# Optimization experiments

Measured on AMD Instinct MI355X. Metric: run time of the kernel, lower is better.

Reference implementation:

```python
import jax, jax.numpy as jnp
import numpy as np

N, IN, OUT, T = 32768, 512, 512, 8


def setup_inputs() -> dict:
    key = jax.random.key(0)
    k1, k2, k3 = jax.random.split(key, 3)
    x = jax.random.normal(k1, (N, IN), dtype=jnp.float32)
    x_type = jax.random.randint(k2, (N,), 0, T, dtype=jnp.int32)
    # xavier_uniform with relu gain, per torch reset_parameters
    gain = np.sqrt(2.0)
    bound = gain * np.sqrt(6.0 / (IN + OUT))
    W = jax.random.uniform(k3, (T, IN, OUT), dtype=jnp.float32,
                           minval=-bound, maxval=bound)
    return {"x": x, "x_type": x_type, "W": W}


def reference(x, x_type, W):
    # gather_mm semantics: out[i] = x[i] @ W[x_type[i]]
    # Expressed as a small fixed loop over types (T=8) with masking, which
    # avoids materializing the [N, IN, OUT] gathered weight tensor.
    num_types = W.shape[0]
    out = jnp.zeros((x.shape[0], W.shape[2]), dtype=x.dtype)
    for t in range(num_types):
        mask = (x_type == t)[:, None]  # [N, 1]
        out = out + jnp.where(mask, x @ W[t], jnp.zeros((), dtype=x.dtype))
    return out
```

## Files before the change

### kernel.cpp

```cpp
#include <hip/hip_runtime.h>
#include <hip/hip_bf16.h>

#define N_ROWS 32768
#define K_DIM 512
#define OUT_DIM 512
#define N_TYPES 8
#define NB 520
#define BM 64
#define BN 256
#define BK 64

typedef __attribute__((ext_vector_type(8))) short bf16x8;
typedef __attribute__((ext_vector_type(4))) float f32x4;

__device__ inline ushort f2bf(float f) {
    __hip_bfloat16 h = __float2bfloat16(f);
    return *reinterpret_cast<ushort*>(&h);
}

__device__ inline void gload_lds16(const void* g, void* l) {
    __builtin_amdgcn_global_load_lds(
        (const __attribute__((address_space(1))) void*)g,
        (__attribute__((address_space(3))) void*)l, 16, 0, 0);
}

__global__ void k_init(int* meta) {
    if (threadIdx.x < 32) meta[threadIdx.x] = 0;
}

__global__ void k_hist(const int* __restrict__ x_type, int* meta) {
    __shared__ int cnt[N_TYPES];
    if (threadIdx.x < N_TYPES) cnt[threadIdx.x] = 0;
    __syncthreads();
    int i = blockIdx.x * 256 + threadIdx.x;
    atomicAdd(&cnt[x_type[i]], 1);
    __syncthreads();
    if (threadIdx.x < N_TYPES && cnt[threadIdx.x] > 0)
        atomicAdd(&meta[threadIdx.x], cnt[threadIdx.x]);
}

__global__ void k_scan(int* meta) {
    if (threadIdx.x == 0) {
        int s = 0;
        for (int t = 0; t < N_TYPES; ++t) {
            meta[8 + t]  = s;
            meta[20 + t] = s;
            s += (meta[t] + 63) & ~63;
        }
        meta[16] = s;
    }
}

__global__ void k_fill(const int* __restrict__ x_type, int* meta, int* __restrict__ row_ids) {
    __shared__ int lcnt[N_TYPES];
    __shared__ int lbase[N_TYPES];
    if (threadIdx.x < N_TYPES) lcnt[threadIdx.x] = 0;
    __syncthreads();
    int i = blockIdx.x * 256 + threadIdx.x;
    int t = x_type[i];
    int lpos = atomicAdd(&lcnt[t], 1);
    __syncthreads();
    if (threadIdx.x < N_TYPES)
        lbase[threadIdx.x] = (lcnt[threadIdx.x] > 0)
            ? atomicAdd(&meta[20 + threadIdx.x], lcnt[threadIdx.x]) : 0;
    __syncthreads();
    row_ids[lbase[t] + lpos] = i;
}

__global__ void k_wt(const float* __restrict__ W, ushort* __restrict__ Wt) {
    __shared__ float tile[64][65];
    int t = blockIdx.x, kb = blockIdx.y, cb = blockIdx.z;
    const float* src = W + (size_t)t * K_DIM * OUT_DIM + (size_t)kb * 64 * OUT_DIM + cb * 64;
    #pragma unroll
    for (int j = 0; j < 16; ++j) {
        int idx = threadIdx.x + j * 256;
        int r = idx >> 6, c = idx & 63;
        tile[r][c] = src[(size_t)r * OUT_DIM + c];
    }
    __syncthreads();
    ushort* dst = Wt + (size_t)t * OUT_DIM * K_DIM + (size_t)(cb * 64) * K_DIM + kb * 64;
    #pragma unroll
    for (int j = 0; j < 16; ++j) {
        int idx = threadIdx.x + j * 256;
        int cc = idx >> 6, kk = idx & 63;
        dst[(size_t)cc * K_DIM + kk] = f2bf(tile[kk][cc]);
    }
}

__global__ __launch_bounds__(512, 6) void k_gemm5(
    const float* __restrict__ x, const ushort* __restrict__ Wt,
    const int* __restrict__ meta, const int* __restrict__ row_ids,
    float* __restrict__ out) {

    __shared__ ushort As[BM * BK];
    __shared__ ushort Bs[BN * BK];
    __shared__ int rids[BM];

    int b = blockIdx.x;
    int r0 = b * BM;
    if (r0 >= meta[16]) return;
    int type = 0;
    #pragma unroll
    for (int t = 0; t < N_TYPES; ++t)
        if (r0 >= meta[8 + t]) type = t;

    int tid = threadIdx.x;
    int wave = tid >> 6, lane = tid & 63;

    if (tid < BM) rids[tid] = row_ids[r0 + tid];
    __syncthreads();

    int c0 = blockIdx.y * BN;
    const ushort* Wtt = Wt + (size_t)type * OUT_DIM * K_DIM + (size_t)c0 * K_DIM;

    int sa_row  = tid >> 3;
    int sa_slot = tid & 7;
    int sa_rid  = rids[sa_row];
    const float* sa_src = x + (size_t)max(sa_rid, 0) * K_DIM + sa_slot * 8;
    int sa_byte = (sa_row * 128 + sa_slot * 16) ^ ((sa_row & 7) << 4);

    int sb_colgrp = lane >> 3;
    int sb_kbyte  = ((lane & 7) * 16) ^ (sb_colgrp << 4);

    int wrb = (wave >> 2) * 32;
    int wcb = (wave & 3) * 64;
    int lrow = lane & 15;
    int lkb16 = (lane >> 4) * 16;

    f32x4 acc[2][4] = {};

    #pragma unroll 1
    for (int kk = 0; kk < K_DIM; kk += BK) {
        #pragma unroll
        for (int j = 0; j < 4; ++j) {
            int chunk = wave * 4 + j;
            int col = chunk * 8 + sb_colgrp;
            gload_lds16(Wtt + (size_t)col * K_DIM + kk + (sb_kbyte >> 1),
                        &Bs[chunk * 512]);
        }
        {
            ushort tmp[8] = {0, 0, 0, 0, 0, 0, 0, 0};
            if (sa_rid >= 0) {
                float4 v0 = *reinterpret_cast<const float4*>(sa_src + kk);
                float4 v1 = *reinterpret_cast<const float4*>(sa_src + kk + 4);
                tmp[0] = f2bf(v0.x); tmp[1] = f2bf(v0.y); tmp[2] = f2bf(v0.z); tmp[3] = f2bf(v0.w);
                tmp[4] = f2bf(v1.x); tmp[5] = f2bf(v1.y); tmp[6] = f2bf(v1.z); tmp[7] = f2bf(v1.w);
            }
            *reinterpret_cast<uint4*>((char*)As + sa_byte) = *reinterpret_cast<const uint4*>(tmp);
        }
        __syncthreads();

        #pragma unroll
        for (int s = 0; s < 2; ++s) {
            bf16x8 af[2], bfr[4];
            #pragma unroll
            for (int mi = 0; mi < 2; ++mi) {
                int row = wrb + mi * 16 + lrow;
                int byte = (row * 128 + s * 64 + lkb16) ^ ((row & 7) << 4);
                af[mi] = *reinterpret_cast<const bf16x8*>((const char*)As + byte);
            }
            #pragma unroll
            for (int ni = 0; ni < 4; ++ni) {
                int col = wcb + ni * 16 + lrow;
                int byte = (col * 128 + s * 64 + lkb16) ^ ((col & 7) << 4);
                bfr[ni] = *reinterpret_cast<const bf16x8*>((const char*)Bs + byte);
            }
            #pragma unroll
            for (int mi = 0; mi < 2; ++mi)
                #pragma unroll
                for (int ni = 0; ni < 4; ++ni)
                    acc[mi][ni] = __builtin_amdgcn_mfma_f32_16x16x32_bf16(
                        af[mi], bfr[ni], acc[mi][ni], 0, 0, 0);
        }
        __syncthreads();
    }

    int rgrp = (lane >> 4) * 4;
    #pragma unroll
    for (int mi = 0; mi < 2; ++mi) {
        #pragma unroll
        for (int rr = 0; rr < 4; ++rr) {
            int lr = wrb + mi * 16 + rgrp + rr;
            int gr = rids[lr];
            if (gr >= 0) {
                float* dst = out + (size_t)gr * OUT_DIM + c0 + wcb;
                #pragma unroll
                for (int ni = 0; ni < 4; ++ni)
                    dst[ni * 16 + lrow] = acc[mi][ni][rr];
            }
        }
    }
}

extern "C" void kernel_launch(void* const* d_in, const int* in_sizes, int n_in,
                              void* d_out, int out_size, void* d_ws, size_t ws_size,
                              hipStream_t stream) {
    const float* x      = (const float*)d_in[0];
    const int*   x_type = (const int*)d_in[1];
    const float* W      = (const float*)d_in[2];
    float* out          = (float*)d_out;

    char* ws = (char*)d_ws;
    size_t off_rids = 256;
    size_t off_wt   = off_rids + sizeof(int) * (NB * 64);
    int* meta    = (int*)ws;
    int* row_ids = (int*)(ws + off_rids);
    ushort* Wt   = (ushort*)(ws + off_wt);

    k_init<<<1, 64, 0, stream>>>(meta);
    k_hist<<<N_ROWS / 256, 256, 0, stream>>>(x_type, meta);
    k_scan<<<1, 64, 0, stream>>>(meta);
    hipMemsetAsync(row_ids, 0xFF, sizeof(int) * (NB * 64), stream);
    k_fill<<<N_ROWS / 256, 256, 0, stream>>>(x_type, meta, row_ids);

    dim3 wgrid(N_TYPES, K_DIM / 64, OUT_DIM / 64);
    k_wt<<<wgrid, 256, 0, stream>>>(W, Wt);

    dim3 ggrid(NB, OUT_DIM / BN);
    k_gemm5<<<ggrid, 512, 0, stream>>>(x, Wt, meta, row_ids, out);
}
```

Before: 64.02 us.

## Double-buffer grouped GEMM tiles, halve column tile, reorder grid for row reuse

```diff
diff --git a/kernel.cpp b/kernel.cpp
--- a/kernel.cpp
+++ b/kernel.cpp
@@ -7,8 +7,9 @@
 #define N_TYPES 8
 #define NB 520
 #define BM 64
-#define BN 256
+#define BN 128
 #define BK 64
+#define NT (K_DIM / BK)
 
 typedef __attribute__((ext_vector_type(8))) short bf16x8;
 typedef __attribute__((ext_vector_type(4))) float f32x4;
@@ -87,16 +88,16 @@
     }
 }
 
-__global__ __launch_bounds__(512, 6) void k_gemm5(
+__global__ __launch_bounds__(512, 4) void k_gemm7(
     const float* __restrict__ x, const ushort* __restrict__ Wt,
     const int* __restrict__ meta, const int* __restrict__ row_ids,
     float* __restrict__ out) {
 
-    __shared__ ushort As[BM * BK];
-    __shared__ ushort Bs[BN * BK];
+    __shared__ ushort As[2 * BM * BK];
+    __shared__ ushort Bs[2 * BN * BK];
     __shared__ int rids[BM];
 
-    int b = blockIdx.x;
+    int b = blockIdx.y;
     int r0 = b * BM;
     if (r0 >= meta[16]) return;
     int type = 0;
@@ -110,7 +111,7 @@
     if (tid < BM) rids[tid] = row_ids[r0 + tid];
     __syncthreads();
 
-    int c0 = blockIdx.y * BN;
+    int c0 = blockIdx.x * BN;
     const ushort* Wtt = Wt + (size_t)type * OUT_DIM * K_DIM + (size_t)c0 * K_DIM;
 
     int sa_row  = tid >> 3;
@@ -120,59 +121,90 @@
     int sa_byte = (sa_row * 128 + sa_slot * 16) ^ ((sa_row & 7) << 4);
 
     int sb_colgrp = lane >> 3;
-    int sb_kbyte  = ((lane & 7) * 16) ^ (sb_colgrp << 4);
+    int sb_koff   = (((lane & 7) * 16) ^ (sb_colgrp << 4)) >> 1;
 
     int wrb = (wave >> 2) * 32;
-    int wcb = (wave & 3) * 64;
+    int wcb = (wave & 3) * 32;
     int lrow = lane & 15;
     int lkb16 = (lane >> 4) * 16;
 
-    f32x4 acc[2][4] = {};
-
-    #pragma unroll 1
-    for (int kk = 0; kk < K_DIM; kk += BK) {
-        #pragma unroll
-        for (int j = 0; j < 4; ++j) {
-            int chunk = wave * 4 + j;
-            int col = chunk * 8 + sb_colgrp;
-            gload_lds16(Wtt + (size_t)col * K_DIM + kk + (sb_kbyte >> 1),
-                        &Bs[chunk * 512]);
-        }
-        {
-            ushort tmp[8] = {0, 0, 0, 0, 0, 0, 0, 0};
+    f32x4 acc[2][2] = {};
+
+#define STAGE_B(buf, kk)                                                        \
+    _Pragma("unroll")                                                           \
+    for (int j = 0; j < 2; ++j) {                                               \
+        int chunk = wave * 2 + j;                                               \
+        int col = chunk * 8 + sb_colgrp;                                        \
+        gload_lds16(Wtt + (size_t)col * K_DIM + (kk) + sb_koff,                 \
+                    (char*)Bs + (buf) * 16384 + chunk * 1024);                  \
+    }
+
+#define WRITE_A(buf, v0, v1)                                                    \
+    {                                                                           \
+        ushort tmp[8] = {0, 0, 0, 0, 0, 0, 0, 0};                               \
+        if (sa_rid >= 0) {                                                      \
+            tmp[0] = f2bf(v0.x); tmp[1] = f2bf(v0.y);                           \
+            tmp[2] = f2bf(v0.z); tmp[3] = f2bf(v0.w);                           \
+            tmp[4] = f2bf(v1.x); tmp[5] = f2bf(v1.y);                           \
+            tmp[6] = f2bf(v1.z); tmp[7] = f2bf(v1.w);                           \
+        }                                                                       \
+        *reinterpret_cast<uint4*>((char*)As + (buf) * 8192 + sa_byte) =         \
+            *reinterpret_cast<const uint4*>(tmp);                               \
+    }
+
+#define COMPUTE(buf)                                                            \
+    _Pragma("unroll")                                                           \
+    for (int s = 0; s < 2; ++s) {                                               \
+        bf16x8 af[2], bfr[2];                                                   \
+        _Pragma("unroll")                                                       \
+        for (int mi = 0; mi < 2; ++mi) {                                        \
+            int row = wrb + mi * 16 + lrow;                                     \
+            int byte = (row * 128 + s * 64 + lkb16) ^ ((row & 7) << 4);         \
+            af[mi] = *reinterpret_cast<const bf16x8*>(                          \
+                (const char*)As + (buf) * 8192 + byte);                         \
+        }                                                                       \
+        _Pragma("unroll")                                                       \
+        for (int ni = 0; ni < 2; ++ni) {                                        \
+            int col = wcb + ni * 16 + lrow;                                     \
+            int byte = (col * 128 + s * 64 + lkb16) ^ ((col & 7) << 4);         \
+            bfr[ni] = *reinterpret_cast<const bf16x8*>(                         \
+                (const char*)Bs + (buf) * 16384 + byte);                        \
+        }                                                                       \
+        _Pragma("unroll")                                                       \
+        for (int mi = 0; mi < 2; ++mi)                                          \
+            _Pragma("unroll")                                                   \
+            for (int ni = 0; ni < 2; ++ni)                                      \
+                acc[mi][ni] = __builtin_amdgcn_mfma_f32_16x16x32_bf16(          \
+                    af[mi], bfr[ni], acc[mi][ni], 0, 0, 0);                     \
+    }
+
+    STAGE_B(0, 0)
+    {
+        float4 v0 = {0,0,0,0}, v1 = {0,0,0,0};
+        if (sa_rid >= 0) {
+            v0 = *reinterpret_cast<const float4*>(sa_src);
+            v1 = *reinterpret_cast<const float4*>(sa_src + 4);
+        }
+        WRITE_A(0, v0, v1)
+    }
+    __syncthreads();
+
+    #pragma unroll 2
+    for (int t = 0; t < NT; ++t) {
+        int cur = t & 1;
+        float4 v0 = {0,0,0,0}, v1 = {0,0,0,0};
+        if (t < NT - 1) {
+            STAGE_B(cur ^ 1, (t + 1) * BK)
             if (sa_rid >= 0) {
-                float4 v0 = *reinterpret_cast<const float4*>(sa_src + kk);
-                float4 v1 = *reinterpret_cast<const float4*>(sa_src + kk + 4);
-                tmp[0] = f2bf(v0.x); tmp[1] = f2bf(v0.y); tmp[2] = f2bf(v0.z); tmp[3] = f2bf(v0.w);
-                tmp[4] = f2bf(v1.x); tmp[5] = f2bf(v1.y); tmp[6] = f2bf(v1.z); tmp[7] = f2bf(v1.w);
+                v0 = *reinterpret_cast<const float4*>(sa_src + (t + 1) * BK);
+                v1 = *reinterpret_cast<const float4*>(sa_src + (t + 1) * BK + 4);
             }
-            *reinterpret_cast<uint4*>((char*)As + sa_byte) = *reinterpret_cast<const uint4*>(tmp);
-        }
-        __syncthreads();
-
-        #pragma unroll
-        for (int s = 0; s < 2; ++s) {
-            bf16x8 af[2], bfr[4];
-            #pragma unroll
-            for (int mi = 0; mi < 2; ++mi) {
-                int row = wrb + mi * 16 + lrow;
-                int byte = (row * 128 + s * 64 + lkb16) ^ ((row & 7) << 4);
-                af[mi] = *reinterpret_cast<const bf16x8*>((const char*)As + byte);
-            }
-            #pragma unroll
-            for (int ni = 0; ni < 4; ++ni) {
-                int col = wcb + ni * 16 + lrow;
-                int byte = (col * 128 + s * 64 + lkb16) ^ ((col & 7) << 4);
-                bfr[ni] = *reinterpret_cast<const bf16x8*>((const char*)Bs + byte);
-            }
-            #pragma unroll
-            for (int mi = 0; mi < 2; ++mi)
-                #pragma unroll
-                for (int ni = 0; ni < 4; ++ni)
-                    acc[mi][ni] = __builtin_amdgcn_mfma_f32_16x16x32_bf16(
-                        af[mi], bfr[ni], acc[mi][ni], 0, 0, 0);
-        }
-        __syncthreads();
+        }
+        COMPUTE(cur)
+        if (t < NT - 1) {
+            WRITE_A(cur ^ 1, v0, v1)
+            __syncthreads();
+        }
     }
 
     int rgrp = (lane >> 4) * 4;
@@ -185,7 +217,7 @@
             if (gr >= 0) {
                 float* dst = out + (size_t)gr * OUT_DIM + c0 + wcb;
                 #pragma unroll
-                for (int ni = 0; ni < 4; ++ni)
+                for (int ni = 0; ni < 2; ++ni)
                     dst[ni * 16 + lrow] = acc[mi][ni][rr];
             }
         }
@@ -216,6 +248,6 @@
     dim3 wgrid(N_TYPES, K_DIM / 64, OUT_DIM / 64);
     k_wt<<<wgrid, 256, 0, stream>>>(W, Wt);
 
-    dim3 ggrid(NB, OUT_DIM / BN);
-    k_gemm5<<<ggrid, 512, 0, stream>>>(x, Wt, meta, row_ids, out);
-}
+    dim3 ggrid(OUT_DIM / BN, NB);
+    k_gemm7<<<ggrid, 512, 0, stream>>>(x, Wt, meta, row_ids, out);
+}
```

Measured after the change: 76.20 us. +19.0%, slower.

## Retile grouped GEMM to 128x128 blocks with 4x4 MFMA per wave

Applied to the files above, without the earlier changes.

```diff
diff --git a/kernel.cpp b/kernel.cpp
--- a/kernel.cpp
+++ b/kernel.cpp
@@ -5,10 +5,10 @@
 #define K_DIM 512
 #define OUT_DIM 512
 #define N_TYPES 8
-#define NB 520
-#define BM 64
-#define BN 256
+#define BMR 128
+#define NBR 264
 #define BK 64
+#define NT (K_DIM / BK)
 
 typedef __attribute__((ext_vector_type(8))) short bf16x8;
 typedef __attribute__((ext_vector_type(4))) float f32x4;
@@ -45,7 +45,7 @@
         for (int t = 0; t < N_TYPES; ++t) {
             meta[8 + t]  = s;
             meta[20 + t] = s;
-            s += (meta[t] + 63) & ~63;
+            s += (meta[t] + BMR - 1) & ~(BMR - 1);
         }
         meta[16] = s;
     }
@@ -87,17 +87,17 @@
     }
 }
 
-__global__ __launch_bounds__(512, 6) void k_gemm5(
+__global__ __launch_bounds__(256) void k_gemm9(
     const float* __restrict__ x, const ushort* __restrict__ Wt,
     const int* __restrict__ meta, const int* __restrict__ row_ids,
     float* __restrict__ out) {
 
-    __shared__ ushort As[BM * BK];
-    __shared__ ushort Bs[BN * BK];
-    __shared__ int rids[BM];
+    __shared__ ushort As[BMR * BK];
+    __shared__ ushort Bs[128 * BK];
+    __shared__ int rids[BMR];
 
     int b = blockIdx.x;
-    int r0 = b * BM;
+    int r0 = b * BMR;
     if (r0 >= meta[16]) return;
     int type = 0;
     #pragma unroll
@@ -107,66 +107,76 @@
     int tid = threadIdx.x;
     int wave = tid >> 6, lane = tid & 63;
 
-    if (tid < BM) rids[tid] = row_ids[r0 + tid];
-    __syncthreads();
-
-    int c0 = blockIdx.y * BN;
+    if (tid < BMR) rids[tid] = row_ids[r0 + tid];
+    __syncthreads();
+
+    int c0 = blockIdx.y * 128;
     const ushort* Wtt = Wt + (size_t)type * OUT_DIM * K_DIM + (size_t)c0 * K_DIM;
 
-    int sa_row  = tid >> 3;
-    int sa_slot = tid & 7;
+    int sa_row  = tid >> 1;
+    int sa_half = tid & 1;
     int sa_rid  = rids[sa_row];
-    const float* sa_src = x + (size_t)max(sa_rid, 0) * K_DIM + sa_slot * 8;
-    int sa_byte = (sa_row * 128 + sa_slot * 16) ^ ((sa_row & 7) << 4);
-
-    int sb_colgrp = lane >> 3;
-    int sb_kbyte  = ((lane & 7) * 16) ^ (sb_colgrp << 4);
-
-    int wrb = (wave >> 2) * 32;
-    int wcb = (wave & 3) * 64;
+    const float* sa_src = x + (size_t)max(sa_rid, 0) * K_DIM + sa_half * 32;
+
+    int sb_col = lane >> 3;
+    int sb_p   = lane & 7;
+    int sb_srcg = sb_p ^ sb_col;
+
+    int wrb = (wave >> 1) * 64;
+    int wcb = (wave & 1) * 64;
     int lrow = lane & 15;
-    int lkb16 = (lane >> 4) * 16;
-
-    f32x4 acc[2][4] = {};
-
-    #pragma unroll 1
-    for (int kk = 0; kk < K_DIM; kk += BK) {
+    int g16  = lane >> 4;
+
+    f32x4 acc[4][4] = {};
+
+    #pragma unroll 2
+    for (int t8 = 0; t8 < NT; ++t8) {
+        int kk = t8 * BK;
         #pragma unroll
         for (int j = 0; j < 4; ++j) {
             int chunk = wave * 4 + j;
-            int col = chunk * 8 + sb_colgrp;
-            gload_lds16(Wtt + (size_t)col * K_DIM + kk + (sb_kbyte >> 1),
-                        &Bs[chunk * 512]);
+            int col = chunk * 8 + sb_col;
+            gload_lds16(Wtt + (size_t)col * K_DIM + kk + sb_srcg * 8,
+                        (char*)Bs + chunk * 1024);
         }
         {
-            ushort tmp[8] = {0, 0, 0, 0, 0, 0, 0, 0};
-            if (sa_rid >= 0) {
-                float4 v0 = *reinterpret_cast<const float4*>(sa_src + kk);
-                float4 v1 = *reinterpret_cast<const float4*>(sa_src + kk + 4);
-                tmp[0] = f2bf(v0.x); tmp[1] = f2bf(v0.y); tmp[2] = f2bf(v0.z); tmp[3] = f2bf(v0.w);
-                tmp[4] = f2bf(v1.x); tmp[5] = f2bf(v1.y); tmp[6] = f2bf(v1.z); tmp[7] = f2bf(v1.w);
-            }
-            *reinterpret_cast<uint4*>((char*)As + sa_byte) = *reinterpret_cast<const uint4*>(tmp);
+            float4 v[8];
+            #pragma unroll
+            for (int q = 0; q < 8; ++q)
+                v[q] = (sa_rid >= 0)
+                    ? *reinterpret_cast<const float4*>(sa_src + kk + q * 4)
+                    : float4{0.f, 0.f, 0.f, 0.f};
+            #pragma unroll
+            for (int q = 0; q < 4; ++q) {
+                ushort tmp[8] = {
+                    f2bf(v[q*2].x),   f2bf(v[q*2].y),   f2bf(v[q*2].z),   f2bf(v[q*2].w),
+                    f2bf(v[q*2+1].x), f2bf(v[q*2+1].y), f2bf(v[q*2+1].z), f2bf(v[q*2+1].w) };
+                int p = sa_half * 4 + q;
+                int byte = sa_row * 128 + ((p ^ (sa_row & 7)) * 16);
+                *reinterpret_cast<uint4*>((char*)As + byte) =
+                    *reinterpret_cast<const uint4*>(tmp);
+            }
         }
         __syncthreads();
 
         #pragma unroll
         for (int s = 0; s < 2; ++s) {
-            bf16x8 af[2], bfr[4];
-            #pragma unroll
-            for (int mi = 0; mi < 2; ++mi) {
+            int g = s * 4 + g16;
+            bf16x8 af[4], bfr[4];
+            #pragma unroll
+            for (int mi = 0; mi < 4; ++mi) {
                 int row = wrb + mi * 16 + lrow;
-                int byte = (row * 128 + s * 64 + lkb16) ^ ((row & 7) << 4);
+                int byte = row * 128 + ((g ^ (row & 7)) * 16);
                 af[mi] = *reinterpret_cast<const bf16x8*>((const char*)As + byte);
             }
             #pragma unroll
             for (int ni = 0; ni < 4; ++ni) {
                 int col = wcb + ni * 16 + lrow;
-                int byte = (col * 128 + s * 64 + lkb16) ^ ((col & 7) << 4);
+                int byte = col * 128 + ((g ^ (col & 7)) * 16);
                 bfr[ni] = *reinterpret_cast<const bf16x8*>((const char*)Bs + byte);
             }
             #pragma unroll
-            for (int mi = 0; mi < 2; ++mi)
+            for (int mi = 0; mi < 4; ++mi)
                 #pragma unroll
                 for (int ni = 0; ni < 4; ++ni)
                     acc[mi][ni] = __builtin_amdgcn_mfma_f32_16x16x32_bf16(
@@ -175,9 +185,9 @@
         __syncthreads();
     }
 
-    int rgrp = (lane >> 4) * 4;
-    #pragma unroll
-    for (int mi = 0; mi < 2; ++mi) {
+    int rgrp = g16 * 4;
+    #pragma unroll
+    for (int mi = 0; mi < 4; ++mi) {
         #pragma unroll
         for (int rr = 0; rr < 4; ++rr) {
             int lr = wrb + mi * 16 + rgrp + rr;
@@ -202,7 +212,7 @@
 
     char* ws = (char*)d_ws;
     size_t off_rids = 256;
-    size_t off_wt   = off_rids + sizeof(int) * (NB * 64);
+    size_t off_wt   = off_rids + sizeof(int) * (NBR * BMR);
     int* meta    = (int*)ws;
     int* row_ids = (int*)(ws + off_rids);
     ushort* Wt   = (ushort*)(ws + off_wt);
@@ -210,12 +220,12 @@
     k_init<<<1, 64, 0, stream>>>(meta);
     k_hist<<<N_ROWS / 256, 256, 0, stream>>>(x_type, meta);
     k_scan<<<1, 64, 0, stream>>>(meta);
-    hipMemsetAsync(row_ids, 0xFF, sizeof(int) * (NB * 64), stream);
+    hipMemsetAsync(row_ids, 0xFF, sizeof(int) * (NBR * BMR), stream);
     k_fill<<<N_ROWS / 256, 256, 0, stream>>>(x_type, meta, row_ids);
 
     dim3 wgrid(N_TYPES, K_DIM / 64, OUT_DIM / 64);
     k_wt<<<wgrid, 256, 0, stream>>>(W, Wt);
 
-    dim3 ggrid(NB, OUT_DIM / BN);
-    k_gemm5<<<ggrid, 512, 0, stream>>>(x, Wt, meta, row_ids, out);
-}
+    dim3 ggrid(NBR, OUT_DIM / 128);
+    k_gemm9<<<ggrid, 256, 0, stream>>>(x, Wt, meta, row_ids, out);
+}
```

New measurement: 116.1 us. 81.4% more time.

## Drop histogram/scan kernels by bucketing rows into fixed per-type slabs

Applied to the files above, without the earlier changes.

```diff
diff --git a/kernel.cpp b/kernel.cpp
--- a/kernel.cpp
+++ b/kernel.cpp
@@ -5,10 +5,10 @@
 #define K_DIM 512
 #define OUT_DIM 512
 #define N_TYPES 8
-#define NB 520
 #define BM 64
 #define BN 256
 #define BK 64
+#define TPB 512
 
 typedef __attribute__((ext_vector_type(8))) short bf16x8;
 typedef __attribute__((ext_vector_type(4))) float f32x4;
@@ -24,33 +24,6 @@
         (__attribute__((address_space(3))) void*)l, 16, 0, 0);
 }
 
-__global__ void k_init(int* meta) {
-    if (threadIdx.x < 32) meta[threadIdx.x] = 0;
-}
-
-__global__ void k_hist(const int* __restrict__ x_type, int* meta) {
-    __shared__ int cnt[N_TYPES];
-    if (threadIdx.x < N_TYPES) cnt[threadIdx.x] = 0;
-    __syncthreads();
-    int i = blockIdx.x * 256 + threadIdx.x;
-    atomicAdd(&cnt[x_type[i]], 1);
-    __syncthreads();
-    if (threadIdx.x < N_TYPES && cnt[threadIdx.x] > 0)
-        atomicAdd(&meta[threadIdx.x], cnt[threadIdx.x]);
-}
-
-__global__ void k_scan(int* meta) {
-    if (threadIdx.x == 0) {
-        int s = 0;
-        for (int t = 0; t < N_TYPES; ++t) {
-            meta[8 + t]  = s;
-            meta[20 + t] = s;
-            s += (meta[t] + 63) & ~63;
-        }
-        meta[16] = s;
-    }
-}
-
 __global__ void k_fill(const int* __restrict__ x_type, int* meta, int* __restrict__ row_ids) {
     __shared__ int lcnt[N_TYPES];
     __shared__ int lbase[N_TYPES];
@@ -62,9 +35,9 @@
     __syncthreads();
     if (threadIdx.x < N_TYPES)
         lbase[threadIdx.x] = (lcnt[threadIdx.x] > 0)
-            ? atomicAdd(&meta[20 + threadIdx.x], lcnt[threadIdx.x]) : 0;
+            ? atomicAdd(&meta[threadIdx.x], lcnt[threadIdx.x]) : 0;
     __syncthreads();
-    row_ids[lbase[t] + lpos] = i;
+    row_ids[(size_t)t * N_ROWS + lbase[t] + lpos] = i;
 }
 
 __global__ void k_wt(const float* __restrict__ W, ushort* __restrict__ Wt) {
@@ -87,7 +60,7 @@
     }
 }
 
-__global__ __launch_bounds__(512, 6) void k_gemm5(
+__global__ __launch_bounds__(512, 4) void k_gemm13(
     const float* __restrict__ x, const ushort* __restrict__ Wt,
     const int* __restrict__ meta, const int* __restrict__ row_ids,
     float* __restrict__ out) {
@@ -97,17 +70,14 @@
     __shared__ int rids[BM];
 
     int b = blockIdx.x;
-    int r0 = b * BM;
-    if (r0 >= meta[16]) return;
-    int type = 0;
-    #pragma unroll
-    for (int t = 0; t < N_TYPES; ++t)
-        if (r0 >= meta[8 + t]) type = t;
+    int type = b >> 9;
+    int r0 = (b & (TPB - 1)) * BM;
+    if (r0 >= meta[type]) return;
 
     int tid = threadIdx.x;
     int wave = tid >> 6, lane = tid & 63;
 
-    if (tid < BM) rids[tid] = row_ids[r0 + tid];
+    if (tid < BM) rids[tid] = row_ids[(size_t)type * N_ROWS + r0 + tid];
     __syncthreads();
 
     int c0 = blockIdx.y * BN;
@@ -120,7 +90,7 @@
     int sa_byte = (sa_row * 128 + sa_slot * 16) ^ ((sa_row & 7) << 4);
 
     int sb_colgrp = lane >> 3;
-    int sb_kbyte  = ((lane & 7) * 16) ^ (sb_colgrp << 4);
+    int sb_koff   = (((lane & 7) * 16) ^ (sb_colgrp << 4)) >> 1;
 
     int wrb = (wave >> 2) * 32;
     int wcb = (wave & 3) * 64;
@@ -135,8 +105,8 @@
         for (int j = 0; j < 4; ++j) {
             int chunk = wave * 4 + j;
             int col = chunk * 8 + sb_colgrp;
-            gload_lds16(Wtt + (size_t)col * K_DIM + kk + (sb_kbyte >> 1),
-                        &Bs[chunk * 512]);
+            gload_lds16(Wtt + (size_t)col * K_DIM + kk + sb_koff,
+                        (char*)Bs + chunk * 1024);
         }
         {
             ushort tmp[8] = {0, 0, 0, 0, 0, 0, 0, 0};
@@ -202,20 +172,18 @@
 
     char* ws = (char*)d_ws;
     size_t off_rids = 256;
-    size_t off_wt   = off_rids + sizeof(int) * (NB * 64);
+    size_t off_wt   = off_rids + sizeof(int) * (size_t)N_TYPES * N_ROWS;
     int* meta    = (int*)ws;
     int* row_ids = (int*)(ws + off_rids);
     ushort* Wt   = (ushort*)(ws + off_wt);
 
-    k_init<<<1, 64, 0, stream>>>(meta);
-    k_hist<<<N_ROWS / 256, 256, 0, stream>>>(x_type, meta);
-    k_scan<<<1, 64, 0, stream>>>(meta);
-    hipMemsetAsync(row_ids, 0xFF, sizeof(int) * (NB * 64), stream);
+    hipMemsetAsync(meta, 0, sizeof(int) * N_TYPES, stream);
+    hipMemsetAsync(row_ids, 0xFF, sizeof(int) * (size_t)N_TYPES * N_ROWS, stream);
     k_fill<<<N_ROWS / 256, 256, 0, stream>>>(x_type, meta, row_ids);
 
     dim3 wgrid(N_TYPES, K_DIM / 64, OUT_DIM / 64);
     k_wt<<<wgrid, 256, 0, stream>>>(W, Wt);
 
-    dim3 ggrid(NB, OUT_DIM / BN);
-    k_gemm5<<<ggrid, 512, 0, stream>>>(x, Wt, meta, row_ids, out);
+    dim3 ggrid(N_TYPES * TPB, OUT_DIM / BN);
+    k_gemm13<<<ggrid, 512, 0, stream>>>(x, Wt, meta, row_ids, out);
 }
```

Measured after the change: 62.12 us. -3.0%, faster.
